# Kernel optimization log

Measured on AMD Instinct MI355X. Metric: run time of the kernel, lower is better.

Reference implementation:

```python
import jax, jax.numpy as jnp
import numpy as np

B, S, T, V, E, H = 32, 64, 64, 32000, 512, 1024


def setup_inputs() -> dict:
    key = jax.random.key(0)
    ks = jax.random.split(key, 12)
    n = lambda k, shp, s=0.05: jax.random.normal(k, shp, dtype=jnp.float32) * s
    return {
        "src": jax.random.randint(ks[0], (B, S), 0, V, dtype=jnp.int32),
        "tgt": jax.random.randint(ks[1], (B, T), 0, V, dtype=jnp.int32),
        "enc_emb": n(ks[2], (V, E)),
        "dec_emb": n(ks[3], (V, E)),
        "Wih_e": n(ks[4], (E, H)), "bih_e": jnp.zeros((H,), jnp.float32),
        "Whh_e": n(ks[5], (H, H)), "bhh_e": jnp.zeros((H,), jnp.float32),
        "Wih_d": n(ks[6], (E, H)), "bih_d": jnp.zeros((H,), jnp.float32),
        "Whh_d": n(ks[7], (H, H)), "bhh_d": jnp.zeros((H,), jnp.float32),
        "Wout": n(ks[8], (H, V)), "bout": jnp.zeros((V,), jnp.float32),
    }


def reference(src, tgt, enc_emb, dec_emb, Wih_e, bih_e, Whh_e, bhh_e,
              Wih_d, bih_d, Whh_d, bhh_d, Wout, bout):
    # Embedding lookups: [B, S, E] / [B, T, E]
    src_e = enc_emb[src]
    tgt_e = dec_emb[tgt]
    # Precompute input-to-hidden projections for every timestep (same math,
    # batched into one GEMM each): [B, S, H] / [B, T, H]
    x_e = jnp.einsum('bse,eh->bsh', src_e, Wih_e) + bih_e
    x_d = jnp.einsum('bte,eh->bth', tgt_e, Wih_d) + bih_d

    h0 = jnp.zeros((src.shape[0], Whh_e.shape[0]), dtype=x_e.dtype)

    def enc_step(h, x):  # h,x: [B, H]
        h = jnp.tanh(x + h @ Whh_e + bhh_e)
        return h, None

    h_enc, _ = jax.lax.scan(enc_step, h0, jnp.swapaxes(x_e, 0, 1))

    def dec_step(h, x):
        h = jnp.tanh(x + h @ Whh_d + bhh_d)
        return h, h

    _, hs = jax.lax.scan(dec_step, h_enc, jnp.swapaxes(x_d, 0, 1))  # [T, B, H]

    logits = jnp.einsum('tbh,hv->tbv', hs, Wout) + bout  # [T, B, V]
    out = jax.nn.log_softmax(logits, axis=-1)
    return jnp.swapaxes(out, 0, 1)  # [B, T, V]
```

## Files before the change

### kernel.cpp

```cpp
#include <hip/hip_runtime.h>
#include <hip/hip_bf16.h>
#include <math.h>

#define B_ 32
#define S_ 64
#define T_ 64
#define V_ 32000
#define E_ 512
#define H_ 1024

typedef __attribute__((ext_vector_type(8))) short short8;
typedef __attribute__((ext_vector_type(4))) float f32x4;

static __device__ __forceinline__ unsigned short f2bf(float f) {
  union { float f; unsigned u; } c; c.f = f;
  unsigned r = (c.u + 0x7fffu + ((c.u >> 16) & 1u)) >> 16;
  return (unsigned short)r;
}

__global__ __launch_bounds__(128)
void gather_f32(const int* __restrict__ idx, const float* __restrict__ emb,
                float* __restrict__ dst) {
  int r = blockIdx.x;
  int tid = threadIdx.x;
  int tok = idx[r];
  float4 v = *(const float4*)(emb + (size_t)tok * E_ + tid * 4);
  *(float4*)(dst + (size_t)r * E_ + tid * 4) = v;
}

__global__ __launch_bounds__(256)
void dgemm_bias(const float* __restrict__ A, const float* __restrict__ B,
                const float* __restrict__ bias, float* __restrict__ C,
                int M, int N, int K) {
  __shared__ float As[32][65];
  __shared__ float Bs[32][64];
  const int nbm = M >> 6;
  const int bm = blockIdx.x % nbm;
  const int bn = blockIdx.x / nbm;
  const int tid = threadIdx.x;
  const int tr = tid >> 4, tc = tid & 15;
  double acc[4][4] = {};

  for (int kt = 0; kt < K; kt += 32) {
    {
      int arow = tid >> 3, acol = (tid & 7) * 4;
#pragma unroll
      for (int p = 0; p < 2; ++p) {
        int r = arow + p * 32;
        float4 v = *(const float4*)(A + (size_t)(bm * 64 + r) * K + kt + acol);
        As[acol + 0][r] = v.x; As[acol + 1][r] = v.y;
        As[acol + 2][r] = v.z; As[acol + 3][r] = v.w;
      }
      int brow = tid >> 4, bcol = (tid & 15) * 4;
#pragma unroll
      for (int p = 0; p < 2; ++p) {
        int r = brow + p * 16;
        float4 v = *(const float4*)(B + (size_t)(kt + r) * N + bn * 64 + bcol);
        *(float4*)(&Bs[r][bcol]) = v;
      }
    }
    __syncthreads();
#pragma unroll
    for (int k = 0; k < 32; ++k) {
      double a[4], b[4];
#pragma unroll
      for (int i = 0; i < 4; ++i) a[i] = (double)As[k][tr * 4 + i];
#pragma unroll
      for (int j = 0; j < 4; ++j) b[j] = (double)Bs[k][tc * 4 + j];
#pragma unroll
      for (int i = 0; i < 4; ++i)
#pragma unroll
        for (int j = 0; j < 4; ++j) acc[i][j] = fma(a[i], b[j], acc[i][j]);
    }
    __syncthreads();
  }
#pragma unroll
  for (int i = 0; i < 4; ++i) {
    int gm = bm * 64 + tr * 4 + i;
    int gn = bn * 64 + tc * 4;
    float4 o;
    o.x = (float)(acc[i][0] + (double)bias[gn + 0]);
    o.y = (float)(acc[i][1] + (double)bias[gn + 1]);
    o.z = (float)(acc[i][2] + (double)bias[gn + 2]);
    o.w = (float)(acc[i][3] + (double)bias[gn + 3]);
    *(float4*)(C + (size_t)gm * N + gn) = o;
  }
}

__global__ __launch_bounds__(256)
void transpose_f32(const float* __restrict__ W, float* __restrict__ WT,
                   int K, int N) {
  __shared__ float t[64][65];
  int k0 = blockIdx.x * 64;
  int n0 = blockIdx.y * 64;
  int tid = threadIdx.x;
  int r = tid >> 4, c4 = tid & 15;
#pragma unroll
  for (int i = 0; i < 4; ++i) {
    int row = r + i * 16;
    float4 v = *(const float4*)(W + (size_t)(k0 + row) * N + n0 + c4 * 4);
    t[row][c4 * 4 + 0] = v.x; t[row][c4 * 4 + 1] = v.y;
    t[row][c4 * 4 + 2] = v.z; t[row][c4 * 4 + 3] = v.w;
  }
  __syncthreads();
#pragma unroll
  for (int i = 0; i < 4; ++i) {
    int n = r + i * 16;
    float4 o;
    o.x = t[c4 * 4 + 0][n]; o.y = t[c4 * 4 + 1][n];
    o.z = t[c4 * 4 + 2][n]; o.w = t[c4 * 4 + 3][n];
    *(float4*)(WT + (size_t)(n0 + n) * K + k0 + c4 * 4) = o;
  }
}

__global__ __launch_bounds__(256)
void transpose_bf16(const float* __restrict__ W, unsigned short* __restrict__ WT,
                    int K, int N) {
  __shared__ float t[64][65];
  int k0 = blockIdx.x * 64;
  int n0 = blockIdx.y * 64;
  int tid = threadIdx.x;
  int r = tid >> 4, c4 = tid & 15;
#pragma unroll
  for (int i = 0; i < 4; ++i) {
    int row = r + i * 16;
    float4 v = *(const float4*)(W + (size_t)(k0 + row) * N + n0 + c4 * 4);
    t[row][c4 * 4 + 0] = v.x; t[row][c4 * 4 + 1] = v.y;
    t[row][c4 * 4 + 2] = v.z; t[row][c4 * 4 + 3] = v.w;
  }
  __syncthreads();
#pragma unroll
  for (int i = 0; i < 4; ++i) {
    int n = r + i * 16;
    ushort4 o;
    o.x = f2bf(t[c4 * 4 + 0][n]); o.y = f2bf(t[c4 * 4 + 1][n]);
    o.z = f2bf(t[c4 * 4 + 2][n]); o.w = f2bf(t[c4 * 4 + 3][n]);
    *(ushort4*)(WT + (size_t)(n0 + n) * K + k0 + c4 * 4) = o;
  }
}

__global__ __launch_bounds__(256)
void gemm_bt_swap(const unsigned short* __restrict__ A, const unsigned short* __restrict__ BT,
                  const float* __restrict__ bias, float* __restrict__ C,
                  int M, int N, int K) {
  __shared__ unsigned short As[128 * 64];
  __shared__ unsigned short Bs[128 * 64];
  const int nbm = M >> 7;
  int idx = blockIdx.x;
  const int cpx = gridDim.x >> 3;
  idx = (idx & 7) * cpx + (idx >> 3);
  const int bm = idx % nbm;
  const int bn = idx / nbm;
  const int tid = threadIdx.x;
  const int lane = tid & 63;
  const int wr = (tid >> 6) >> 1;
  const int wc = (tid >> 6) & 1;

  f32x4 acc[4][4] = {};

  for (int kt = 0; kt < K; kt += 64) {
#pragma unroll
    for (int i = 0; i < 4; ++i) {
      int c = i * 256 + tid;
      int row = c >> 3, col8 = c & 7;
      int sw = col8 ^ (row & 7);
      short8 av = *(const short8*)(A + (size_t)(bm * 128 + row) * K + kt + col8 * 8);
      short8 bv = *(const short8*)(BT + (size_t)(bn * 128 + row) * K + kt + col8 * 8);
      *(short8*)(As + row * 64 + sw * 8) = av;
      *(short8*)(Bs + row * 64 + sw * 8) = bv;
    }
    __syncthreads();
#pragma unroll
    for (int kk = 0; kk < 64; kk += 32) {
      int kc = (kk + ((lane >> 4) << 3)) >> 3;
      short8 af[4], bfr[4];
#pragma unroll
      for (int mi = 0; mi < 4; ++mi) {
        int row = wr * 64 + mi * 16 + (lane & 15);
        af[mi] = *(const short8*)(As + row * 64 + ((kc ^ (row & 7)) << 3));
      }
#pragma unroll
      for (int ni = 0; ni < 4; ++ni) {
        int row = wc * 64 + ni * 16 + (lane & 15);
        bfr[ni] = *(const short8*)(Bs + row * 64 + ((kc ^ (row & 7)) << 3));
      }
#pragma unroll
      for (int mi = 0; mi < 4; ++mi)
#pragma unroll
        for (int ni = 0; ni < 4; ++ni)
          acc[mi][ni] = __builtin_amdgcn_mfma_f32_16x16x32_bf16(
              af[mi], bfr[ni], acc[mi][ni], 0, 0, 0);
    }
    __syncthreads();
  }

  const int cq = (lane >> 4) << 2;
  const int cn = lane & 15;
#pragma unroll
  for (int mi = 0; mi < 4; ++mi) {
#pragma unroll
    for (int ni = 0; ni < 4; ++ni) {
      int gn = bn * 128 + wc * 64 + ni * 16 + cn;
      float bv = bias[gn];
#pragma unroll
      for (int q = 0; q < 4; ++q) {
        int gm = bm * 128 + wr * 64 + mi * 16 + cq + q;
        int b = gm & (B_ - 1);
        int t = gm >> 5;
        __builtin_nontemporal_store(acc[mi][ni][q] + bv,
                                    &C[((size_t)b * T_ + t) * N + gn]);
      }
    }
  }
}

__global__ __launch_bounds__(512)
void rnn_scan_grp2(const float* __restrict__ xe, const float* __restrict__ xd,
                   const float* __restrict__ WTe, const float* __restrict__ WTd,
                   const float* __restrict__ bhhE, const float* __restrict__ bhhD,
                   float* __restrict__ hA, float* __restrict__ hB,
                   unsigned short* __restrict__ hsb, unsigned* __restrict__ bar) {
  __shared__ float hl[4 * 1024];
  const int tid = threadIdx.x;
  const int grp = blockIdx.x & 7;
  const int jslot = blockIdx.x >> 3;
  const int jbase = jslot * 32;
  const int bg = grp * 4;
  const int w = tid >> 6;
  const int l = tid & 63;
  unsigned* mybar = bar + grp * 32;

  const int a = 8 * (l & 1) + 4 * ((l >> 1) & 1) + 2 * ((l >> 2) & 1) +
                ((l >> 3) & 1);
  const int lb = a >> 2;
  const int gb = bg + lb;
  const int gj = jbase + w * 4 + (a & 3);
  const float bje = bhhE[gj];
  const float bjd = bhhD[gj];

  float4 wreg[4][4];
  {
    const float* wsrc = WTe + (size_t)(jbase + w * 4) * 1024;
#pragma unroll
    for (int i = 0; i < 4; ++i) {
      int g = l + 64 * i;
#pragma unroll
      for (int ji = 0; ji < 4; ++ji)
        wreg[i][ji] = *(const float4*)(wsrc + (size_t)ji * 1024 + g * 4);
    }
  }

  for (int t = 0; t < 128; ++t) {
    if (t == 64) {
      const float* wsrc = WTd + (size_t)(jbase + w * 4) * 1024;
#pragma unroll
      for (int i = 0; i < 4; ++i) {
        int g = l + 64 * i;
#pragma unroll
        for (int ji = 0; ji < 4; ++ji)
          wreg[i][ji] = *(const float4*)(wsrc + (size_t)ji * 1024 + g * 4);
      }
    }
    const bool enc = (t < 64);
    const int s = t & 63;
    const float* __restrict__ h_in = (t & 1) ? hB : hA;
    float* __restrict__ h_out = (t & 1) ? hA : hB;
    const float* __restrict__ x = enc ? xe : xd;

    float xv = x[((size_t)gb * 64 + s) * H_ + gj];

    {
      const float* hsrc = h_in + bg * H_;
      float v[8];
#pragma unroll
      for (int u = 0; u < 8; ++u)
        v[u] = __hip_atomic_load(hsrc + u * 512 + tid, __ATOMIC_RELAXED,
                                 __HIP_MEMORY_SCOPE_AGENT);
#pragma unroll
      for (int u = 0; u < 8; ++u)
        hl[u * 512 + tid] = v[u];
    }
    __syncthreads();

    double acc[4][4];
#pragma unroll
    for (int bi = 0; bi < 4; ++bi)
#pragma unroll
      for (int ji = 0; ji < 4; ++ji) acc[bi][ji] = 0.;

#pragma unroll
    for (int i = 0; i < 4; ++i) {
      int g = l + 64 * i;
      float4 hv[4];
#pragma unroll
      for (int bi = 0; bi < 4; ++bi)
        hv[bi] = *(const float4*)(hl + bi * 1024 + g * 4);
#pragma unroll
      for (int bi = 0; bi < 4; ++bi)
#pragma unroll
        for (int ji = 0; ji < 4; ++ji) {
          acc[bi][ji] = fma((double)hv[bi].x, (double)wreg[i][ji].x, acc[bi][ji]);
          acc[bi][ji] = fma((double)hv[bi].y, (double)wreg[i][ji].y, acc[bi][ji]);
          acc[bi][ji] = fma((double)hv[bi].z, (double)wreg[i][ji].z, acc[bi][ji]);
          acc[bi][ji] = fma((double)hv[bi].w, (double)wreg[i][ji].w, acc[bi][ji]);
        }
    }

    double r8[8], r4[4], r2[2], r1;
#pragma unroll
    for (int aa = 0; aa < 8; ++aa) {
      double send = (l & 1) ? acc[aa >> 2][aa & 3] : acc[(aa + 8) >> 2][(aa + 8) & 3];
      double mine = (l & 1) ? acc[(aa + 8) >> 2][(aa + 8) & 3] : acc[aa >> 2][aa & 3];
      r8[aa] = mine + __shfl_xor(send, 1);
    }
#pragma unroll
    for (int aa = 0; aa < 4; ++aa) {
      double send = (l & 2) ? r8[aa] : r8[aa + 4];
      double mine = (l & 2) ? r8[aa + 4] : r8[aa];
      r4[aa] = mine + __shfl_xor(send, 2);
    }
#pragma unroll
    for (int aa = 0; aa < 2; ++aa) {
      double send = (l & 4) ? r4[aa] : r4[aa + 2];
      double mine = (l & 4) ? r4[aa + 2] : r4[aa];
      r2[aa] = mine + __shfl_xor(send, 4);
    }
    {
      double send = (l & 8) ? r2[0] : r2[1];
      double mine = (l & 8) ? r2[1] : r2[0];
      r1 = mine + __shfl_xor(send, 8);
    }
    r1 += __shfl_xor(r1, 16);
    r1 += __shfl_xor(r1, 32);

    if (l < 16) {
      double v = r1 + (double)xv + (double)(enc ? bje : bjd);
      double h = tanh(v);
      float hf = (float)h;
      __hip_atomic_store(&h_out[(size_t)gb * H_ + gj], hf, __ATOMIC_RELAXED,
                         __HIP_MEMORY_SCOPE_AGENT);
      if (!enc)
        __builtin_nontemporal_store(f2bf(hf),
                                    &hsb[(size_t)s * (B_ * H_) + gb * H_ + gj]);
    }

    if (t < 127) {
      asm volatile("s_waitcnt vmcnt(0)" ::: "memory");
      __syncthreads();
      if (tid == 0) {
        __hip_atomic_fetch_add(mybar, 1u, __ATOMIC_RELAXED,
                               __HIP_MEMORY_SCOPE_AGENT);
        unsigned tgt = 32u * (unsigned)(t + 1);
        while (__hip_atomic_load(mybar, __ATOMIC_RELAXED,
                                 __HIP_MEMORY_SCOPE_AGENT) < tgt)
          __builtin_amdgcn_s_sleep(1);
      }
      __syncthreads();
    }
  }
}

__global__ __launch_bounds__(512)
void log_softmax_rows(float* __restrict__ out) {
  __shared__ float rl[32000];
  __shared__ float wm[8], wsv[8];
  float* row = out + (size_t)blockIdx.x * V_;
  const int tid = threadIdx.x;
  float m = -INFINITY, s = 0.f;
  for (int i = tid; i < V_ / 4; i += 512) {
    float4 v = *(const float4*)(row + i * 4);
    *(float4*)(rl + i * 4) = v;
    float mx = fmaxf(fmaxf(v.x, v.y), fmaxf(v.z, v.w));
    if (mx > m) { s *= __expf(m - mx); m = mx; }
    s += __expf(v.x - m) + __expf(v.y - m) + __expf(v.z - m) + __expf(v.w - m);
  }
#pragma unroll
  for (int o = 32; o; o >>= 1) {
    float mo = __shfl_xor(m, o);
    float so = __shfl_xor(s, o);
    float mn = fmaxf(m, mo);
    s = s * __expf(m - mn) + so * __expf(mo - mn);
    m = mn;
  }
  int wv = tid >> 6;
  if ((tid & 63) == 0) { wm[wv] = m; wsv[wv] = s; }
  __syncthreads();
  float M = wm[0];
#pragma unroll
  for (int i = 1; i < 8; ++i) M = fmaxf(M, wm[i]);
  float Ssum = 0.f;
#pragma unroll
  for (int i = 0; i < 8; ++i) Ssum += wsv[i] * __expf(wm[i] - M);
  float L = M + logf(Ssum);
  for (int i = tid; i < V_ / 4; i += 512) {
    float4 v = *(const float4*)(rl + i * 4);
    v.x -= L; v.y -= L; v.z -= L; v.w -= L;
    __builtin_nontemporal_store(v.x, &row[i * 4 + 0]);
    __builtin_nontemporal_store(v.y, &row[i * 4 + 1]);
    __builtin_nontemporal_store(v.z, &row[i * 4 + 2]);
    __builtin_nontemporal_store(v.w, &row[i * 4 + 3]);
  }
}

extern "C" void kernel_launch(void* const* d_in, const int* in_sizes, int n_in,
                              void* d_out, int out_size, void* d_ws, size_t ws_size,
                              hipStream_t stream) {
  const int*   src  = (const int*)  d_in[0];
  const int*   tgt  = (const int*)  d_in[1];
  const float* encE = (const float*)d_in[2];
  const float* decE = (const float*)d_in[3];
  const float* WihE = (const float*)d_in[4];
  const float* bihE = (const float*)d_in[5];
  const float* WhhE = (const float*)d_in[6];
  const float* bhhE = (const float*)d_in[7];
  const float* WihD = (const float*)d_in[8];
  const float* bihD = (const float*)d_in[9];
  const float* WhhD = (const float*)d_in[10];
  const float* bhhD = (const float*)d_in[11];
  const float* Wout = (const float*)d_in[12];
  const float* bout = (const float*)d_in[13];
  float* out = (float*)d_out;

  char* w = (char*)d_ws;
  float* x_e = (float*)w;                      w += (size_t)2048 * 1024 * 4;
  float* x_d = (float*)w;                      w += (size_t)2048 * 1024 * 4;
  float* h0  = (float*)w;                      w += 32 * 1024 * 4;
  float* h1  = (float*)w;                      w += 32 * 1024 * 4;
  unsigned* bar = (unsigned*)w;                w += 8 * 32 * 4;
  float* WhhTe = (float*)w;                    w += (size_t)1024 * 1024 * 4;
  float* WhhTd = (float*)w;                    w += (size_t)1024 * 1024 * 4;
  float* AembF = (float*)w;                    w += (size_t)2048 * 512 * 4;
  unsigned short* hsb   = (unsigned short*)w;  w += (size_t)2048 * 1024 * 2;
  unsigned short* WoutT = (unsigned short*)w;  w += (size_t)V_ * 1024 * 2;

  gather_f32<<<B_ * S_, 128, 0, stream>>>(src, encE, AembF);
  dgemm_bias<<<(2048 / 64) * (H_ / 64), 256, 0, stream>>>(AembF, WihE, bihE, x_e,
                                                          2048, H_, E_);
  gather_f32<<<B_ * T_, 128, 0, stream>>>(tgt, decE, AembF);
  dgemm_bias<<<(2048 / 64) * (H_ / 64), 256, 0, stream>>>(AembF, WihD, bihD, x_d,
                                                          2048, H_, E_);

  transpose_f32<<<dim3(H_ / 64, H_ / 64), 256, 0, stream>>>(WhhE, WhhTe, H_, H_);
  transpose_f32<<<dim3(H_ / 64, H_ / 64), 256, 0, stream>>>(WhhD, WhhTd, H_, H_);

  hipMemsetAsync(h0, 0, 32 * 1024 * 4, stream);
  hipMemsetAsync(bar, 0, 8 * 32 * 4, stream);
  rnn_scan_grp2<<<256, 512, 0, stream>>>(x_e, x_d, WhhTe, WhhTd, bhhE, bhhD,
                                         h0, h1, hsb, bar);

  transpose_bf16<<<dim3(H_ / 64, V_ / 64), 256, 0, stream>>>(Wout, WoutT, H_, V_);
  gemm_bt_swap<<<(2048 / 128) * (V_ / 128), 256, 0, stream>>>(hsb, WoutT, bout, out,
                                                              2048, V_, H_);
  log_softmax_rows<<<B_ * T_, 512, 0, stream>>>(out);
}
```

Before: 1.128 ms.

## Fuse embedding gather into input GEMM, prefetch logits tiles, widen softmax blocks

The embedding gather now happens inside the input-projection GEMM, which removes two gather launches and the intermediate buffer. The shared-memory reads in that GEMM become float4 loads. The bf16 output GEMM register-prefetches the next K tile from global memory while the current tile is being computed. The decoder's bf16 hidden-state store moves after the grid barrier so it stays off the critical path. Log-softmax now runs with 1024 threads per row, which raises per-row parallelism but may lower occupancy given the large shared-memory footprint.

```diff
diff --git a/kernel.cpp b/kernel.cpp
--- a/kernel.cpp
+++ b/kernel.cpp
@@ -18,36 +18,34 @@
   return (unsigned short)r;
 }
 
-__global__ __launch_bounds__(128)
-void gather_f32(const int* __restrict__ idx, const float* __restrict__ emb,
-                float* __restrict__ dst) {
-  int r = blockIdx.x;
-  int tid = threadIdx.x;
-  int tok = idx[r];
-  float4 v = *(const float4*)(emb + (size_t)tok * E_ + tid * 4);
-  *(float4*)(dst + (size_t)r * E_ + tid * 4) = v;
-}
-
 __global__ __launch_bounds__(256)
-void dgemm_bias(const float* __restrict__ A, const float* __restrict__ B,
-                const float* __restrict__ bias, float* __restrict__ C,
-                int M, int N, int K) {
-  __shared__ float As[32][65];
+void dgemm_embed(const int* __restrict__ idx, const float* __restrict__ emb,
+                 const float* __restrict__ B, const float* __restrict__ bias,
+                 float* __restrict__ C, int M, int N, int K) {
+  __shared__ float As[32][68];
   __shared__ float Bs[32][64];
   const int nbm = M >> 6;
   const int bm = blockIdx.x % nbm;
   const int bn = blockIdx.x / nbm;
   const int tid = threadIdx.x;
   const int tr = tid >> 4, tc = tid & 15;
+
+  const int arow = tid >> 3, acol = (tid & 7) * 4;
+  const float* arp[2];
+#pragma unroll
+  for (int p = 0; p < 2; ++p) {
+    int r = arow + p * 32;
+    arp[p] = emb + (size_t)idx[bm * 64 + r] * E_;
+  }
+
   double acc[4][4] = {};
 
   for (int kt = 0; kt < K; kt += 32) {
     {
-      int arow = tid >> 3, acol = (tid & 7) * 4;
 #pragma unroll
       for (int p = 0; p < 2; ++p) {
         int r = arow + p * 32;
-        float4 v = *(const float4*)(A + (size_t)(bm * 64 + r) * K + kt + acol);
+        float4 v = *(const float4*)(arp[p] + kt + acol);
         As[acol + 0][r] = v.x; As[acol + 1][r] = v.y;
         As[acol + 2][r] = v.z; As[acol + 3][r] = v.w;
       }
@@ -62,11 +60,10 @@
     __syncthreads();
 #pragma unroll
     for (int k = 0; k < 32; ++k) {
-      double a[4], b[4];
-#pragma unroll
-      for (int i = 0; i < 4; ++i) a[i] = (double)As[k][tr * 4 + i];
-#pragma unroll
-      for (int j = 0; j < 4; ++j) b[j] = (double)Bs[k][tc * 4 + j];
+      float4 av = *(const float4*)(&As[k][tr * 4]);
+      float4 bv = *(const float4*)(&Bs[k][tc * 4]);
+      double a[4] = {(double)av.x, (double)av.y, (double)av.z, (double)av.w};
+      double b[4] = {(double)bv.x, (double)bv.y, (double)bv.z, (double)bv.w};
 #pragma unroll
       for (int i = 0; i < 4; ++i)
 #pragma unroll
@@ -158,18 +155,37 @@
 
   f32x4 acc[4][4] = {};
 
+  int srow[4], scol8[4], ssw[4];
+#pragma unroll
+  for (int i = 0; i < 4; ++i) {
+    int c = i * 256 + tid;
+    srow[i] = c >> 3; scol8[i] = c & 7;
+    ssw[i] = scol8[i] ^ (srow[i] & 7);
+  }
+
+  short8 av[4], bv[4];
+#pragma unroll
+  for (int i = 0; i < 4; ++i) {
+    av[i] = *(const short8*)(A + (size_t)(bm * 128 + srow[i]) * K + scol8[i] * 8);
+    bv[i] = *(const short8*)(BT + (size_t)(bn * 128 + srow[i]) * K + scol8[i] * 8);
+  }
+
   for (int kt = 0; kt < K; kt += 64) {
 #pragma unroll
     for (int i = 0; i < 4; ++i) {
-      int c = i * 256 + tid;
-      int row = c >> 3, col8 = c & 7;
-      int sw = col8 ^ (row & 7);
-      short8 av = *(const short8*)(A + (size_t)(bm * 128 + row) * K + kt + col8 * 8);
-      short8 bv = *(const short8*)(BT + (size_t)(bn * 128 + row) * K + kt + col8 * 8);
-      *(short8*)(As + row * 64 + sw * 8) = av;
-      *(short8*)(Bs + row * 64 + sw * 8) = bv;
+      *(short8*)(As + srow[i] * 64 + ssw[i] * 8) = av[i];
+      *(short8*)(Bs + srow[i] * 64 + ssw[i] * 8) = bv[i];
     }
     __syncthreads();
+
+    if (kt + 64 < K) {
+#pragma unroll
+      for (int i = 0; i < 4; ++i) {
+        av[i] = *(const short8*)(A + (size_t)(bm * 128 + srow[i]) * K + kt + 64 + scol8[i] * 8);
+        bv[i] = *(const short8*)(BT + (size_t)(bn * 128 + srow[i]) * K + kt + 64 + scol8[i] * 8);
+      }
+    }
+
 #pragma unroll
     for (int kk = 0; kk < 64; kk += 32) {
       int kc = (kk + ((lane >> 4) << 3)) >> 3;
@@ -201,13 +217,13 @@
 #pragma unroll
     for (int ni = 0; ni < 4; ++ni) {
       int gn = bn * 128 + wc * 64 + ni * 16 + cn;
-      float bv = bias[gn];
+      float bvv = bias[gn];
 #pragma unroll
       for (int q = 0; q < 4; ++q) {
         int gm = bm * 128 + wr * 64 + mi * 16 + cq + q;
         int b = gm & (B_ - 1);
         int t = gm >> 5;
-        __builtin_nontemporal_store(acc[mi][ni][q] + bv,
+        __builtin_nontemporal_store(acc[mi][ni][q] + bvv,
                                     &C[((size_t)b * T_ + t) * N + gn]);
       }
     }
@@ -333,15 +349,13 @@
     r1 += __shfl_xor(r1, 16);
     r1 += __shfl_xor(r1, 32);
 
+    float hf = 0.f;
     if (l < 16) {
       double v = r1 + (double)xv + (double)(enc ? bje : bjd);
       double h = tanh(v);
-      float hf = (float)h;
+      hf = (float)h;
       __hip_atomic_store(&h_out[(size_t)gb * H_ + gj], hf, __ATOMIC_RELAXED,
                          __HIP_MEMORY_SCOPE_AGENT);
-      if (!enc)
-        __builtin_nontemporal_store(f2bf(hf),
-                                    &hsb[(size_t)s * (B_ * H_) + gb * H_ + gj]);
     }
 
     if (t < 127) {
@@ -357,17 +371,20 @@
       }
       __syncthreads();
     }
-  }
-}
-
-__global__ __launch_bounds__(512)
+    if (!enc && l < 16)
+      __builtin_nontemporal_store(f2bf(hf),
+                                  &hsb[(size_t)s * (B_ * H_) + (size_t)gb * H_ + gj]);
+  }
+}
+
+__global__ __launch_bounds__(1024)
 void log_softmax_rows(float* __restrict__ out) {
   __shared__ float rl[32000];
-  __shared__ float wm[8], wsv[8];
+  __shared__ float wm[16], wsv[16];
   float* row = out + (size_t)blockIdx.x * V_;
   const int tid = threadIdx.x;
   float m = -INFINITY, s = 0.f;
-  for (int i = tid; i < V_ / 4; i += 512) {
+  for (int i = tid; i < V_ / 4; i += 1024) {
     float4 v = *(const float4*)(row + i * 4);
     *(float4*)(rl + i * 4) = v;
     float mx = fmaxf(fmaxf(v.x, v.y), fmaxf(v.z, v.w));
@@ -387,12 +404,12 @@
   __syncthreads();
   float M = wm[0];
 #pragma unroll
-  for (int i = 1; i < 8; ++i) M = fmaxf(M, wm[i]);
+  for (int i = 1; i < 16; ++i) M = fmaxf(M, wm[i]);
   float Ssum = 0.f;
 #pragma unroll
-  for (int i = 0; i < 8; ++i) Ssum += wsv[i] * __expf(wm[i] - M);
+  for (int i = 0; i < 16; ++i) Ssum += wsv[i] * __expf(wm[i] - M);
   float L = M + logf(Ssum);
-  for (int i = tid; i < V_ / 4; i += 512) {
+  for (int i = tid; i < V_ / 4; i += 1024) {
     float4 v = *(const float4*)(rl + i * 4);
     v.x -= L; v.y -= L; v.z -= L; v.w -= L;
     __builtin_nontemporal_store(v.x, &row[i * 4 + 0]);
@@ -429,16 +446,13 @@
   unsigned* bar = (unsigned*)w;                w += 8 * 32 * 4;
   float* WhhTe = (float*)w;                    w += (size_t)1024 * 1024 * 4;
   float* WhhTd = (float*)w;                    w += (size_t)1024 * 1024 * 4;
-  float* AembF = (float*)w;                    w += (size_t)2048 * 512 * 4;
   unsigned short* hsb   = (unsigned short*)w;  w += (size_t)2048 * 1024 * 2;
   unsigned short* WoutT = (unsigned short*)w;  w += (size_t)V_ * 1024 * 2;
 
-  gather_f32<<<B_ * S_, 128, 0, stream>>>(src, encE, AembF);
-  dgemm_bias<<<(2048 / 64) * (H_ / 64), 256, 0, stream>>>(AembF, WihE, bihE, x_e,
-                                                          2048, H_, E_);
-  gather_f32<<<B_ * T_, 128, 0, stream>>>(tgt, decE, AembF);
-  dgemm_bias<<<(2048 / 64) * (H_ / 64), 256, 0, stream>>>(AembF, WihD, bihD, x_d,
-                                                          2048, H_, E_);
+  dgemm_embed<<<(2048 / 64) * (H_ / 64), 256, 0, stream>>>(src, encE, WihE, bihE,
+                                                           x_e, 2048, H_, E_);
+  dgemm_embed<<<(2048 / 64) * (H_ / 64), 256, 0, stream>>>(tgt, decE, WihD, bihD,
+                                                           x_d, 2048, H_, E_);
 
   transpose_f32<<<dim3(H_ / 64, H_ / 64), 256, 0, stream>>>(WhhE, WhhTe, H_, H_);
   transpose_f32<<<dim3(H_ / 64, H_ / 64), 256, 0, stream>>>(WhhD, WhhTd, H_, H_);
@@ -451,5 +465,5 @@
   transpose_bf16<<<dim3(H_ / 64, V_ / 64), 256, 0, stream>>>(Wout, WoutT, H_, V_);
   gemm_bt_swap<<<(2048 / 128) * (V_ / 128), 256, 0, stream>>>(hsb, WoutT, bout, out,
                                                               2048, V_, H_);
-  log_softmax_rows<<<B_ * T_, 512, 0, stream>>>(out);
-}
+  log_softmax_rows<<<B_ * T_, 1024, 0, stream>>>(out);
+}
```

After: 1.022 ms. 1.1x faster.
